# Optimization experiments

Measured on AMD Instinct MI355X. Metric: run time of the kernel, lower is better.

The kernel has to match this reference:

```python
import jax, jax.numpy as jnp
import numpy as np

DIM = 768
HEADS = 12
D_HEAD = DIM // HEADS
SCALE = DIM ** (-0.5)  # note: full dimension, matching original code


def setup_inputs() -> dict:
    key = jax.random.key(0)
    k1, k2, k3, k4 = jax.random.split(key, 4)
    x = jax.random.normal(k1, (8, 1024, DIM), dtype=jnp.float32)
    w_in = jax.random.normal(k2, (DIM, 3 * DIM), dtype=jnp.float32) * (DIM ** -0.5)
    w_out = jax.random.normal(k3, (DIM, DIM), dtype=jnp.float32) * (DIM ** -0.5)
    b_out = jax.random.normal(k4, (DIM,), dtype=jnp.float32) * 0.01
    return {"x": x, "w_in": w_in, "w_out": w_out, "b_out": b_out}


def reference(x, w_in, w_out, b_out):
    b, n, _ = x.shape
    qkv = x @ w_in  # [b, n, 3*dim]
    # 'b n (qkv h d) -> qkv b h n d'
    qkv = qkv.reshape(b, n, 3, HEADS, D_HEAD).transpose(2, 0, 3, 1, 4)
    q, k, v = qkv[0], qkv[1], qkv[2]
    scores = jnp.einsum('bhid,bhjd->bhij', q, k) * SCALE
    attn = jax.nn.softmax(scores, axis=-1)
    out = jnp.einsum('bhij,bhjd->bhid', attn, v)  # [b, h, n, d]
    out = out.transpose(0, 2, 1, 3).reshape(b, n, DIM)  # 'b h n d -> b n (h d)'
    return out @ w_out + b_out
```

## Files before the change

kernel.cpp:

```cpp
#include <hip/hip_runtime.h>


using short8 = __attribute__((ext_vector_type(8))) short;
using f32x4  = __attribute__((ext_vector_type(4))) float;

#define MFMA_B16(a, b, c) __builtin_amdgcn_mfma_f32_16x16x32_bf16((a), (b), (c), 0, 0, 0)

typedef const __attribute__((address_space(1))) void* gvoid_p;
typedef __attribute__((address_space(3))) void* lvoid_p;

constexpr int   kDim   = 768;
constexpr int   kHeads = 12;
constexpr int   kSeq   = 1024;
constexpr float kScale = 0.03608439182435161f;
constexpr float kQSc   = kScale * 1.4426950408889634f;

__device__ __forceinline__ short f2bf(float f) {
  unsigned u = __float_as_uint(f);
  u += 0x7FFFu + ((u >> 16) & 1u);
  return (short)(u >> 16);
}
__device__ __forceinline__ unsigned cvt_pk_bf16(float lo, float hi) {
  unsigned r;
  asm("v_cvt_pk_bf16_f32 %0, %1, %2" : "=v"(r) : "v"(lo), "v"(hi));
  return r;
}
union U8 { unsigned u[4]; short8 s; };

__global__ __launch_bounds__(256) void prep_kernel(const float* __restrict__ x,
                                                   short* __restrict__ xbf,
                                                   const float* __restrict__ w_in,
                                                   short* __restrict__ WinT,
                                                   const float* __restrict__ w_out,
                                                   short* __restrict__ WoutT) {
  __shared__ float tile[32][33];
  const int bid = blockIdx.x;
  if (bid < 3072) {
    const int i = bid * 256 + threadIdx.x;
    float4 a = ((const float4*)x)[i * 2];
    float4 b = ((const float4*)x)[i * 2 + 1];
    short8 s;
    s[0] = f2bf(a.x); s[1] = f2bf(a.y); s[2] = f2bf(a.z); s[3] = f2bf(a.w);
    s[4] = f2bf(b.x); s[5] = f2bf(b.y); s[6] = f2bf(b.z); s[7] = f2bf(b.w);
    ((short8*)xbf)[i] = s;
    return;
  }
  const float* in; short* out; int R, C, bx, by;
  if (bid < 3072 + 1728) {
    const int b2 = bid - 3072;
    in = w_in; out = WinT; R = 768; C = 2304; bx = b2 % 72; by = b2 / 72;
  } else {
    const int b2 = bid - 4800;
    in = w_out; out = WoutT; R = 768; C = 768; bx = b2 % 24; by = b2 / 24;
  }
  const int c0 = bx * 32, r0 = by * 32;
  const int tx = threadIdx.x & 31, ty = threadIdx.x >> 5;
#pragma unroll
  for (int i = 0; i < 32; i += 8)
    tile[ty + i][tx] = in[(size_t)(r0 + ty + i) * C + c0 + tx];
  __syncthreads();
#pragma unroll
  for (int i = 0; i < 32; i += 8)
    out[(size_t)(c0 + ty + i) * R + r0 + tx] = f2bf(tile[tx][ty + i]);
}

template <int EPI>
__global__ __launch_bounds__(256) void gemm_tile(const short* __restrict__ A,
                                                 const short* __restrict__ BT,
                                                 int Kd,
                                                 short* __restrict__ Qb,
                                                 short* __restrict__ Kb,
                                                 short* __restrict__ VTb,
                                                 const float* __restrict__ bias,
                                                 float* __restrict__ outF) {
  __shared__ short As[3][128 * 32];
  __shared__ short Bs[3][128 * 32];

  const int tid  = threadIdx.x;
  const int lane = tid & 63, w = tid >> 6;
  const int L = lane & 15, g = lane >> 4;
  const int wr = w >> 1, wc = w & 1;
  const int m0 = blockIdx.x * 128, n0 = blockIdx.y * 128;

  const int r4 = lane >> 2;
  const int c8 = (lane & 3) * 8;

  auto stage = [&](int buf, int k0) {
#pragma unroll
    for (int c = 0; c < 2; ++c) {
      const short* ag = A  + (size_t)(m0 + w * 32 + c * 16 + r4) * Kd + k0 + c8;
      const short* bg = BT + (size_t)(n0 + w * 32 + c * 16 + r4) * Kd + k0 + c8;
      __builtin_amdgcn_global_load_lds((gvoid_p)ag, (lvoid_p)&As[buf][(w * 2 + c) * 512], 16, 0, 0);
      __builtin_amdgcn_global_load_lds((gvoid_p)bg, (lvoid_p)&Bs[buf][(w * 2 + c) * 512], 16, 0, 0);
    }
  };

  f32x4 acc[4][4] = {};

  stage(0, 0);
  stage(1, 32);

  const int NT = Kd / 32;
  for (int t = 0; t < NT; ++t) {
    const int cur = t % 3;
    if (t + 2 < NT) stage((t + 2) % 3, (t + 2) * 32);

    if (t + 2 < NT)      asm volatile("s_waitcnt vmcnt(8)" ::: "memory");
    else if (t + 1 < NT) asm volatile("s_waitcnt vmcnt(4)" ::: "memory");
    else                 asm volatile("s_waitcnt vmcnt(0)" ::: "memory");
    __builtin_amdgcn_s_barrier();

    short8 af[4], bfr[4];
#pragma unroll
    for (int mi = 0; mi < 4; ++mi)
      af[mi] = *(const short8*)&As[cur][(wr * 64 + mi * 16 + L) * 32 + g * 8];
#pragma unroll
    for (int ni = 0; ni < 4; ++ni)
      bfr[ni] = *(const short8*)&Bs[cur][(wc * 64 + ni * 16 + L) * 32 + g * 8];
#pragma unroll
    for (int mi = 0; mi < 4; ++mi)
#pragma unroll
      for (int ni = 0; ni < 4; ++ni)
        acc[mi][ni] = MFMA_B16(af[mi], bfr[ni], acc[mi][ni]);

    asm volatile("" ::: "memory");
    __builtin_amdgcn_s_barrier();
  }

  if (EPI == 0) {
    const int t3 = n0 / kDim;
#pragma unroll
    for (int mi = 0; mi < 4; ++mi) {
#pragma unroll
      for (int ni = 0; ni < 4; ++ni) {
        const int gcol = n0 + wc * 64 + ni * 16 + L;
        const int hd = gcol % kDim;
        const int h = hd >> 6, d = hd & 63;
        if (t3 == 2) {
          const int grow = m0 + wr * 64 + mi * 16 + 4 * g;
          const int b = grow >> 10, seq = grow & 1023;
          const int bh = b * kHeads + h;
          const int s6 = seq & 63;
          const int p  = 32 * (s6 >> 5) + 8 * ((s6 >> 2) & 3) + 4 * ((s6 >> 4) & 1);
          const int seqp = (seq & ~63) | p;
          uint2 d2;
          d2.x = cvt_pk_bf16(acc[mi][ni][0], acc[mi][ni][1]);
          d2.y = cvt_pk_bf16(acc[mi][ni][2], acc[mi][ni][3]);
          *(uint2*)&VTb[((size_t)bh * 64 + d) * kSeq + seqp] = d2;
        } else {
#pragma unroll
          for (int r = 0; r < 4; ++r) {
            const int grow = m0 + wr * 64 + mi * 16 + 4 * g + r;
            const int b = grow >> 10, seq = grow & 1023;
            const int bh = b * kHeads + h;
            if (t3 == 0) Qb[((size_t)bh * kSeq + seq) * 64 + d] = f2bf(acc[mi][ni][r] * kQSc);
            else         Kb[((size_t)bh * kSeq + seq) * 64 + d] = f2bf(acc[mi][ni][r]);
          }
        }
      }
    }
  } else {
#pragma unroll
    for (int ni = 0; ni < 4; ++ni) {
      const int gcol = n0 + wc * 64 + ni * 16 + L;
      const float bv = bias[gcol];
#pragma unroll
      for (int mi = 0; mi < 4; ++mi) {
#pragma unroll
        for (int r = 0; r < 4; ++r) {
          const int grow = m0 + wr * 64 + mi * 16 + 4 * g + r;
          outF[(size_t)grow * kDim + gcol] = acc[mi][ni][r] + bv;
        }
      }
    }
  }
}

__global__ __launch_bounds__(256) void attn_kernel(const short* __restrict__ Qb,
                                                   const short* __restrict__ Kb,
                                                   const short* __restrict__ VTb,
                                                   short* __restrict__ AO) {
  __shared__ short Ks[2][64 * 72];
  __shared__ short VTs[2][64 * 72];

  const int tid  = threadIdx.x;
  const int lane = tid & 63, w = tid >> 6;
  const int L = lane & 15, g = lane >> 4;
  const int id = blockIdx.x;
  const int bh = id % 96, qc = id / 96;
  const int q0 = qc * 128 + w * 32;

  const short* Qbase = Qb  + (size_t)bh * kSeq * 64;
  const short* Kbase = Kb  + (size_t)bh * kSeq * 64;
  const short* Vbase = VTb + (size_t)bh * 64 * kSeq;

  short8 qf[2][2];
#pragma unroll
  for (int qh = 0; qh < 2; ++qh) {
    const short* qp = Qbase + (size_t)(q0 + qh * 16 + L) * 64 + g * 8;
    qf[qh][0] = *(const short8*)qp;
    qf[qh][1] = *(const short8*)(qp + 32);
  }

  f32x4 o[2][4] = {};
  float m_[2] = {-1e30f, -1e30f};
  float l_[2] = {0.f, 0.f};

  const int srow = tid >> 2, sc0 = (tid & 3) * 16;

  {
    const short* ksrc = Kbase + (size_t)srow * 64 + sc0;
    const short* vsrc = Vbase + (size_t)srow * kSeq + sc0;
    uint4 k0 = ((const uint4*)ksrc)[0], k1 = ((const uint4*)ksrc)[1];
    uint4 v0 = ((const uint4*)vsrc)[0], v1 = ((const uint4*)vsrc)[1];
    *(uint4*)&Ks[0][srow * 72 + sc0]      = k0;
    *(uint4*)&Ks[0][srow * 72 + sc0 + 8]  = k1;
    *(uint4*)&VTs[0][srow * 72 + sc0]     = v0;
    *(uint4*)&VTs[0][srow * 72 + sc0 + 8] = v1;
  }
  __syncthreads();

  for (int t = 0; t < kSeq / 64; ++t) {
    const int cur = t & 1;
    const bool pf = (t + 1 < kSeq / 64);

    uint4 kr0, kr1, vr0, vr1;
    if (pf) {
      const int kv1 = (t + 1) * 64;
      const short* ksrc = Kbase + (size_t)(kv1 + srow) * 64 + sc0;
      const short* vsrc = Vbase + (size_t)srow * kSeq + kv1 + sc0;
      kr0 = ((const uint4*)ksrc)[0]; kr1 = ((const uint4*)ksrc)[1];
      vr0 = ((const uint4*)vsrc)[0]; vr1 = ((const uint4*)vsrc)[1];
    }

    short8 kf[4][2];
#pragma unroll
    for (int nf = 0; nf < 4; ++nf) {
      const short* kp = &Ks[cur][(nf * 16 + L) * 72 + g * 8];
      kf[nf][0] = *(const short8*)kp;
      kf[nf][1] = *(const short8*)(kp + 32);
    }
    short8 vb[4][2];
#pragma unroll
    for (int nf = 0; nf < 4; ++nf) {
      const short* vrow = &VTs[cur][(nf * 16 + L) * 72];
      vb[nf][0] = *(const short8*)&vrow[g * 8];
      vb[nf][1] = *(const short8*)&vrow[32 + g * 8];
    }

    f32x4 s2[2][4];
    __builtin_amdgcn_s_setprio(1);
#pragma unroll
    for (int qh = 0; qh < 2; ++qh) {
#pragma unroll
      for (int nf = 0; nf < 4; ++nf) {
        f32x4 z = {};
        z = MFMA_B16(kf[nf][0], qf[qh][0], z);
        s2[qh][nf] = MFMA_B16(kf[nf][1], qf[qh][1], z);
      }
    }
    __builtin_amdgcn_s_setprio(0);

#pragma unroll
    for (int qh = 0; qh < 2; ++qh) {
      f32x4* s = s2[qh];
      float x0 = fmaxf(fmaxf(s[0][0], s[0][1]), fmaxf(s[0][2], s[0][3]));
      float x1 = fmaxf(fmaxf(s[1][0], s[1][1]), fmaxf(s[1][2], s[1][3]));
      float x2 = fmaxf(fmaxf(s[2][0], s[2][1]), fmaxf(s[2][2], s[2][3]));
      float x3 = fmaxf(fmaxf(s[3][0], s[3][1]), fmaxf(s[3][2], s[3][3]));
      const float mt4 = fmaxf(fmaxf(x0, x1), fmaxf(x2, x3));

      if (__any(mt4 > m_[qh] + 8.0f)) {
        float mt = fmaxf(mt4, __shfl_xor(mt4, 16, 64));
        mt = fmaxf(mt, __shfl_xor(mt, 32, 64));
        const float mnew = fmaxf(m_[qh], mt);
        const float al = __builtin_amdgcn_exp2f(m_[qh] - mnew);
        m_[qh] = mnew;
        l_[qh] *= al;
        float alr[4];
#pragma unroll
        for (int r = 0; r < 4; ++r) alr[r] = __shfl(al, 4 * g + r, 64);
#pragma unroll
        for (int nf = 0; nf < 4; ++nf)
#pragma unroll
          for (int r = 0; r < 4; ++r) o[qh][nf][r] *= alr[r];
      }

      float rs0 = 0.f, rs1 = 0.f, rs2 = 0.f, rs3 = 0.f;
#pragma unroll
      for (int nf = 0; nf < 4; ++nf) {
        float p0 = __builtin_amdgcn_exp2f(s[nf][0] - m_[qh]);
        float p1 = __builtin_amdgcn_exp2f(s[nf][1] - m_[qh]);
        float p2 = __builtin_amdgcn_exp2f(s[nf][2] - m_[qh]);
        float p3 = __builtin_amdgcn_exp2f(s[nf][3] - m_[qh]);
        s[nf][0] = p0; s[nf][1] = p1; s[nf][2] = p2; s[nf][3] = p3;
        rs0 += p0; rs1 += p1; rs2 += p2; rs3 += p3;
      }
      l_[qh] += (rs0 + rs1) + (rs2 + rs3);

      U8 t0, t1;
      t0.u[0] = cvt_pk_bf16(s[0][0], s[0][1]);
      t0.u[1] = cvt_pk_bf16(s[0][2], s[0][3]);
      t0.u[2] = cvt_pk_bf16(s[1][0], s[1][1]);
      t0.u[3] = cvt_pk_bf16(s[1][2], s[1][3]);
      t1.u[0] = cvt_pk_bf16(s[2][0], s[2][1]);
      t1.u[1] = cvt_pk_bf16(s[2][2], s[2][3]);
      t1.u[2] = cvt_pk_bf16(s[3][0], s[3][1]);
      t1.u[3] = cvt_pk_bf16(s[3][2], s[3][3]);

      __builtin_amdgcn_s_setprio(1);
#pragma unroll
      for (int nf = 0; nf < 4; ++nf) {
        o[qh][nf] = MFMA_B16(t0.s, vb[nf][0], o[qh][nf]);
        o[qh][nf] = MFMA_B16(t1.s, vb[nf][1], o[qh][nf]);
      }
      __builtin_amdgcn_s_setprio(0);
    }

    if (pf) {
      *(uint4*)&Ks[cur ^ 1][srow * 72 + sc0]      = kr0;
      *(uint4*)&Ks[cur ^ 1][srow * 72 + sc0 + 8]  = kr1;
      *(uint4*)&VTs[cur ^ 1][srow * 72 + sc0]     = vr0;
      *(uint4*)&VTs[cur ^ 1][srow * 72 + sc0 + 8] = vr1;
    }
    __syncthreads();
  }

  const int b = bh / kHeads, h = bh % kHeads;
#pragma unroll
  for (int qh = 0; qh < 2; ++qh) {
    float ls = l_[qh] + __shfl_xor(l_[qh], 16, 64);
    ls += __shfl_xor(ls, 32, 64);
    float lq[4];
#pragma unroll
    for (int r = 0; r < 4; ++r) lq[r] = __shfl(ls, 4 * g + r, 64);
    short* aop = AO + ((size_t)(b * kSeq) + q0 + qh * 16) * kDim + h * 64;
#pragma unroll
    for (int r = 0; r < 4; ++r) {
      const float inv = 1.0f / lq[r];
#pragma unroll
      for (int nf = 0; nf < 4; ++nf)
        aop[(size_t)(4 * g + r) * kDim + nf * 16 + L] = f2bf(o[qh][nf][r] * inv);
    }
  }
}

extern "C" void kernel_launch(void* const* d_in, const int* in_sizes, int n_in,
                              void* d_out, int out_size, void* d_ws, size_t ws_size,
                              hipStream_t stream) {
  const float* x     = (const float*)d_in[0];
  const float* w_in  = (const float*)d_in[1];
  const float* w_out = (const float*)d_in[2];
  const float* b_out = (const float*)d_in[3];
  float* out = (float*)d_out;

  short* WinT  = (short*)d_ws;
  short* WoutT = WinT  + (size_t)2304 * 768;
  short* Qb    = WoutT + (size_t)768 * 768;
  short* Kb    = Qb    + (size_t)96 * 1024 * 64;
  short* VTb   = Kb    + (size_t)96 * 1024 * 64;
  short* AO    = VTb   + (size_t)96 * 1024 * 64;
  short* xbf   = AO;

  prep_kernel<<<dim3(3072 + 1728 + 576), 256, 0, stream>>>(
      x, xbf, w_in, WinT, w_out, WoutT);

  gemm_tile<0><<<dim3(8192 / 128, 2304 / 128), 256, 0, stream>>>(
      xbf, WinT, 768, Qb, Kb, VTb, nullptr, nullptr);

  attn_kernel<<<dim3(768), 256, 0, stream>>>(Qb, Kb, VTb, AO);

  gemm_tile<1><<<dim3(8192 / 128, 768 / 128), 256, 0, stream>>>(
      AO, WoutT, 768, nullptr, nullptr, nullptr, b_out, out);
}
```

Measured before the change: 120.0 us.

## Fuse fp32-to-bf16 conversion of x into QKV GEMM A-tile loading

Removes the separate x conversion pass from the prep kernel and instead has the QKV projection GEMM load fp32 x directly into registers, convert with packed bf16 conversion, and store to LDS in a software-pipelined loop. This eliminates a full write and reread of the bf16 copy of x and shrinks the prep launch. In exchange, each column-block of the GEMM rereads fp32 x (double the bytes of bf16), the A path no longer uses direct global-to-LDS loads, and register pressure and wait-count bookkeeping grow.

```diff
diff --git a/kernel.cpp b/kernel.cpp
--- a/kernel.cpp
+++ b/kernel.cpp
@@ -27,30 +27,17 @@
 }
 union U8 { unsigned u[4]; short8 s; };
 
-__global__ __launch_bounds__(256) void prep_kernel(const float* __restrict__ x,
-                                                   short* __restrict__ xbf,
-                                                   const float* __restrict__ w_in,
+__global__ __launch_bounds__(256) void prep_kernel(const float* __restrict__ w_in,
                                                    short* __restrict__ WinT,
                                                    const float* __restrict__ w_out,
                                                    short* __restrict__ WoutT) {
   __shared__ float tile[32][33];
   const int bid = blockIdx.x;
-  if (bid < 3072) {
-    const int i = bid * 256 + threadIdx.x;
-    float4 a = ((const float4*)x)[i * 2];
-    float4 b = ((const float4*)x)[i * 2 + 1];
-    short8 s;
-    s[0] = f2bf(a.x); s[1] = f2bf(a.y); s[2] = f2bf(a.z); s[3] = f2bf(a.w);
-    s[4] = f2bf(b.x); s[5] = f2bf(b.y); s[6] = f2bf(b.z); s[7] = f2bf(b.w);
-    ((short8*)xbf)[i] = s;
-    return;
-  }
   const float* in; short* out; int R, C, bx, by;
-  if (bid < 3072 + 1728) {
-    const int b2 = bid - 3072;
-    in = w_in; out = WinT; R = 768; C = 2304; bx = b2 % 72; by = b2 / 72;
+  if (bid < 1728) {
+    in = w_in; out = WinT; R = 768; C = 2304; bx = bid % 72; by = bid / 72;
   } else {
-    const int b2 = bid - 4800;
+    const int b2 = bid - 1728;
     in = w_out; out = WoutT; R = 768; C = 768; bx = b2 % 24; by = b2 / 24;
   }
   const int c0 = bx * 32, r0 = by * 32;
@@ -64,8 +51,9 @@
     out[(size_t)(c0 + ty + i) * R + r0 + tx] = f2bf(tile[tx][ty + i]);
 }
 
-template <int EPI>
-__global__ __launch_bounds__(256) void gemm_tile(const short* __restrict__ A,
+template <int AMODE, int EPI>
+__global__ __launch_bounds__(256) void gemm_tile(const float* __restrict__ Af,
+                                                 const short* __restrict__ A,
                                                  const short* __restrict__ BT,
                                                  int Kd,
                                                  short* __restrict__ Qb,
@@ -85,31 +73,28 @@
   const int r4 = lane >> 2;
   const int c8 = (lane & 3) * 8;
 
-  auto stage = [&](int buf, int k0) {
+  const int arow = tid >> 1;
+  const int ac16 = (tid & 1) * 16;
+
+  auto stageB = [&](int buf, int k0) {
 #pragma unroll
     for (int c = 0; c < 2; ++c) {
-      const short* ag = A  + (size_t)(m0 + w * 32 + c * 16 + r4) * Kd + k0 + c8;
       const short* bg = BT + (size_t)(n0 + w * 32 + c * 16 + r4) * Kd + k0 + c8;
+      __builtin_amdgcn_global_load_lds((gvoid_p)bg, (lvoid_p)&Bs[buf][(w * 2 + c) * 512], 16, 0, 0);
+    }
+  };
+  auto stageA1 = [&](int buf, int k0) {
+#pragma unroll
+    for (int c = 0; c < 2; ++c) {
+      const short* ag = A + (size_t)(m0 + w * 32 + c * 16 + r4) * Kd + k0 + c8;
       __builtin_amdgcn_global_load_lds((gvoid_p)ag, (lvoid_p)&As[buf][(w * 2 + c) * 512], 16, 0, 0);
-      __builtin_amdgcn_global_load_lds((gvoid_p)bg, (lvoid_p)&Bs[buf][(w * 2 + c) * 512], 16, 0, 0);
     }
   };
 
   f32x4 acc[4][4] = {};
-
-  stage(0, 0);
-  stage(1, 32);
-
   const int NT = Kd / 32;
-  for (int t = 0; t < NT; ++t) {
-    const int cur = t % 3;
-    if (t + 2 < NT) stage((t + 2) % 3, (t + 2) * 32);
-
-    if (t + 2 < NT)      asm volatile("s_waitcnt vmcnt(8)" ::: "memory");
-    else if (t + 1 < NT) asm volatile("s_waitcnt vmcnt(4)" ::: "memory");
-    else                 asm volatile("s_waitcnt vmcnt(0)" ::: "memory");
-    __builtin_amdgcn_s_barrier();
-
+
+  auto compute = [&](int cur) {
     short8 af[4], bfr[4];
 #pragma unroll
     for (int mi = 0; mi < 4; ++mi)
@@ -122,9 +107,72 @@
 #pragma unroll
       for (int ni = 0; ni < 4; ++ni)
         acc[mi][ni] = MFMA_B16(af[mi], bfr[ni], acc[mi][ni]);
-
-    asm volatile("" ::: "memory");
+  };
+
+  if constexpr (AMODE == 1) {
+    stageA1(0, 0); stageB(0, 0);
+    stageA1(1, 32); stageB(1, 32);
+    for (int t = 0; t < NT; ++t) {
+      const int cur = t % 3;
+      if (t + 2 < NT) { stageA1((t + 2) % 3, (t + 2) * 32); stageB((t + 2) % 3, (t + 2) * 32); }
+      if (t + 2 < NT)      asm volatile("s_waitcnt vmcnt(8)" ::: "memory");
+      else if (t + 1 < NT) asm volatile("s_waitcnt vmcnt(4)" ::: "memory");
+      else                 asm volatile("s_waitcnt vmcnt(0)" ::: "memory");
+      __builtin_amdgcn_s_barrier();
+      compute(cur);
+      asm volatile("" ::: "memory");
+      __builtin_amdgcn_s_barrier();
+    }
+  } else {
+    float4 F0[4], F1[4];
+    stageB(0, 0);
+    stageB(1, 32);
+    {
+      const float* ap1 = Af + (size_t)(m0 + arow) * Kd + 32 + ac16;
+      F1[0] = ((const float4*)ap1)[0]; F1[1] = ((const float4*)ap1)[1];
+      F1[2] = ((const float4*)ap1)[2]; F1[3] = ((const float4*)ap1)[3];
+      const float* ap0 = Af + (size_t)(m0 + arow) * Kd + ac16;
+      F0[0] = ((const float4*)ap0)[0]; F0[1] = ((const float4*)ap0)[1];
+      F0[2] = ((const float4*)ap0)[2]; F0[3] = ((const float4*)ap0)[3];
+      uint4 d0, d1;
+      d0.x = cvt_pk_bf16(F0[0].x, F0[0].y); d0.y = cvt_pk_bf16(F0[0].z, F0[0].w);
+      d0.z = cvt_pk_bf16(F0[1].x, F0[1].y); d0.w = cvt_pk_bf16(F0[1].z, F0[1].w);
+      d1.x = cvt_pk_bf16(F0[2].x, F0[2].y); d1.y = cvt_pk_bf16(F0[2].z, F0[2].w);
+      d1.z = cvt_pk_bf16(F0[3].x, F0[3].y); d1.w = cvt_pk_bf16(F0[3].z, F0[3].w);
+      short* dst = &As[0][arow * 32 + ac16];
+      *(uint4*)dst = d0; *(uint4*)(dst + 8) = d1;
+    }
+    asm volatile("s_waitcnt vmcnt(0) lgkmcnt(0)" ::: "memory");
     __builtin_amdgcn_s_barrier();
+
+    auto body = [&](int t, float4 (&Fl)[4], float4 (&Fu)[4]) {
+      if (t + 2 < NT) {
+        stageB((t + 2) % 3, (t + 2) * 32);
+        const float* ap = Af + (size_t)(m0 + arow) * Kd + (t + 2) * 32 + ac16;
+        Fl[0] = ((const float4*)ap)[0]; Fl[1] = ((const float4*)ap)[1];
+        Fl[2] = ((const float4*)ap)[2]; Fl[3] = ((const float4*)ap)[3];
+      }
+      if (t + 1 < NT) {
+        uint4 d0, d1;
+        d0.x = cvt_pk_bf16(Fu[0].x, Fu[0].y); d0.y = cvt_pk_bf16(Fu[0].z, Fu[0].w);
+        d0.z = cvt_pk_bf16(Fu[1].x, Fu[1].y); d0.w = cvt_pk_bf16(Fu[1].z, Fu[1].w);
+        d1.x = cvt_pk_bf16(Fu[2].x, Fu[2].y); d1.y = cvt_pk_bf16(Fu[2].z, Fu[2].w);
+        d1.z = cvt_pk_bf16(Fu[3].x, Fu[3].y); d1.w = cvt_pk_bf16(Fu[3].z, Fu[3].w);
+        short* dst = &As[(t + 1) % 3][arow * 32 + ac16];
+        *(uint4*)dst = d0; *(uint4*)(dst + 8) = d1;
+      }
+      if (t + 2 < NT) asm volatile("s_waitcnt vmcnt(6)" ::: "memory");
+      else            asm volatile("s_waitcnt vmcnt(0)" ::: "memory");
+      asm volatile("s_waitcnt lgkmcnt(0)" ::: "memory");
+      __builtin_amdgcn_s_barrier();
+      compute(t % 3);
+      asm volatile("" ::: "memory");
+      __builtin_amdgcn_s_barrier();
+    };
+    for (int t = 0; t < NT; t += 2) {
+      body(t, F0, F1);
+      body(t + 1, F1, F0);
+    }
   }
 
   if (EPI == 0) {
@@ -360,16 +408,14 @@
   short* Kb    = Qb    + (size_t)96 * 1024 * 64;
   short* VTb   = Kb    + (size_t)96 * 1024 * 64;
   short* AO    = VTb   + (size_t)96 * 1024 * 64;
-  short* xbf   = AO;
-
-  prep_kernel<<<dim3(3072 + 1728 + 576), 256, 0, stream>>>(
-      x, xbf, w_in, WinT, w_out, WoutT);
-
-  gemm_tile<0><<<dim3(8192 / 128, 2304 / 128), 256, 0, stream>>>(
-      xbf, WinT, 768, Qb, Kb, VTb, nullptr, nullptr);
+
+  prep_kernel<<<dim3(1728 + 576), 256, 0, stream>>>(w_in, WinT, w_out, WoutT);
+
+  gemm_tile<0, 0><<<dim3(8192 / 128, 2304 / 128), 256, 0, stream>>>(
+      x, nullptr, WinT, 768, Qb, Kb, VTb, nullptr, nullptr);
 
   attn_kernel<<<dim3(768), 256, 0, stream>>>(Qb, Kb, VTb, AO);
 
-  gemm_tile<1><<<dim3(8192 / 128, 768 / 128), 256, 0, stream>>>(
-      AO, WoutT, 768, nullptr, nullptr, nullptr, b_out, out);
-}
+  gemm_tile<1, 1><<<dim3(8192 / 128, 768 / 128), 256, 0, stream>>>(
+      nullptr, AO, WoutT, 768, nullptr, nullptr, nullptr, b_out, out);
+}
```

After: 148.9 us. 1.24x slower.
